# Optimization experiments

Measured on AMD Instinct MI355X. Metric: run time of the kernel, lower is better.

Reference implementation:

```python
import jax, jax.numpy as jnp
from jax import lax
import numpy as np

B, S, E = 512, 128, 300
NF = 100          # filters per kernel size
NUM_CLASSES = 5


def setup_inputs() -> dict:
    key = jax.random.key(0)
    ks = jax.random.split(key, 9)
    def w(k, shape, fan_in):
        bound = 1.0 / np.sqrt(fan_in)
        return jax.random.uniform(k, shape, jnp.float32, -bound, bound)
    return {
        "x":   jax.random.normal(ks[0], (B, 1, S, E), jnp.float32),
        # conv weights: [out_ch=NF, in_ch=1, kh, kw=E] (the 100 separate 1-channel
        # convs of each kernel size are stacked into one grouped weight tensor)
        "w3": w(ks[1], (NF, 1, 3, E), 3 * E),
        "b3": w(ks[2], (NF,), 3 * E),
        "w4": w(ks[3], (NF, 1, 4, E), 4 * E),
        "b4": w(ks[4], (NF,), 4 * E),
        "w5": w(ks[5], (NF, 1, 5, E), 5 * E),
        "b5": w(ks[6], (NF,), 5 * E),
        "Wfc": w(ks[7], (NUM_CLASSES, 3 * NF), 3 * NF),
        "bfc": w(ks[8], (NUM_CLASSES,), 3 * NF),
    }


def _branch(x, w, b, pad):
    # conv over [B,1,S,E] with kernel [NF,1,k,E]; width fully consumed -> out [B,NF,S',1]
    y = lax.conv_general_dilated(
        x, w, window_strides=(1, 1), padding=[(pad, pad), (0, 0)],
        dimension_numbers=("NCHW", "OIHW", "NCHW"))
    y = jax.nn.relu(y + b[None, :, None, None])
    # relu then global max-pool over the length dim == max over (S', 1)
    return jnp.max(y, axis=(2, 3))  # [B, NF]


def reference(x, w3, b3, w4, b4, w5, b5, Wfc, bfc):
    feats = jnp.concatenate(
        [_branch(x, w3, b3, 0),   # k=3, no padding
         _branch(x, w4, b4, 1),   # k=4, padding (1,0)
         _branch(x, w5, b5, 2)],  # k=5, padding (2,0)
        axis=1)                   # [B, 300]
    logits = feats @ Wfc.T + bfc  # dropout is identity in eval mode
    return jax.nn.log_softmax(logits, axis=1)
```

## Files before the change

kernel.cpp:

```cpp
#include <hip/hip_runtime.h>

typedef __bf16 bf16x8 __attribute__((ext_vector_type(8)));
typedef float  f32x4  __attribute__((ext_vector_type(4)));
typedef unsigned short u16;

#define NB    512
#define SEQ   128
#define EMB   300
#define NT_TOT 19
#define KT_TOT 50
#define WU_ELEMS (304 * 1600)
#define OFF_FEATS (WU_ELEMS * 2)

#define GRP_ELEMS 128000

#define AROW 640
#define A_BYTES (69 * AROW)

__device__ __forceinline__ u16 f2bf(float f) {
  unsigned u = __builtin_bit_cast(unsigned, f);
  return (u16)((u + 0x7fffu + ((u >> 16) & 1u)) >> 16);
}

__global__ void prep_weights(const float* __restrict__ w3, const float* __restrict__ w4,
                             const float* __restrict__ w5, u16* __restrict__ wu) {
  int idx = blockIdx.x * blockDim.x + threadIdx.x;
  if (idx >= WU_ELEMS) return;
  int j = idx & 7, l = (idx >> 3) & 63, t = idx >> 9;
  int nt = t % NT_TOT, kt = t / NT_TOT;
  int f  = nt * 16 + (l & 15);
  int kk = kt * 32 + ((l >> 4) << 3) + j;
  int dk = kk / 320, e = kk - dk * 320;
  float v = 0.f;
  if (f < 300 && e < 300) {
    if (f < 100)      { if (dk >= 2) v = w3[(f * 3 + dk - 2) * 300 + e]; }
    else if (f < 200) { if (dk >= 1) v = w4[((f - 100) * 4 + dk - 1) * 300 + e]; }
    else              {              v = w5[((f - 200) * 5 + dk) * 300 + e]; }
  }
  int g    = nt / 5;
  int tloc = nt - g * 5;
  int ntw  = (g == 3) ? 4 : 5;
  wu[g * GRP_ELEMS + (kt * ntw + tloc) * 512 + (l << 3) + j] = f2bf(v);
}

template<int NTW>
__device__ __forceinline__ void kloop_epi(const char* xs, const char* gB0,
                                          int ntb, int l, int b, int s0,
                                          const float* __restrict__ b3,
                                          const float* __restrict__ b4,
                                          const float* __restrict__ b5,
                                          float* __restrict__ feats) {
  const int lo = l & 15, hi = l >> 4;

  f32x4 acc[4][NTW];
  #pragma unroll
  for (int mt = 0; mt < 4; ++mt)
    #pragma unroll
    for (int j = 0; j < NTW; ++j) acc[mt][j] = (f32x4){0.f, 0.f, 0.f, 0.f};

  bf16x8 aa[4], bC[NTW], bN[NTW];

  const char* gB = gB0 + l * 16;
  #pragma unroll
  for (int j = 0; j < NTW; ++j) bC[j] = *reinterpret_cast<const bf16x8*>(gB + j * 1024);
  #pragma unroll
  for (int j = 0; j < NTW; ++j) bN[j] = *reinterpret_cast<const bf16x8*>(gB + (NTW + j) * 1024);
  gB += 2 * NTW * 1024;

  int abase[4];
  #pragma unroll
  for (int mt = 0; mt < 4; ++mt) abase[mt] = (mt * 16 + lo) * AROW + hi * 16;

#define STEP(AOFF, SW, Bcon) {                                                 \
    _Pragma("unroll") for (int mt = 0; mt < 4; ++mt)                           \
      aa[mt] = *reinterpret_cast<const bf16x8*>(xs + ((abase[mt] + (AOFF)) ^ (SW))); \
    _Pragma("unroll") for (int mt = 0; mt < 4; ++mt)                           \
    _Pragma("unroll") for (int j = 0; j < NTW; ++j)                            \
      acc[mt][j] = __builtin_amdgcn_mfma_f32_16x16x32_bf16(aa[mt], Bcon[j],    \
                                                           acc[mt][j], 0, 0, 0); \
    _Pragma("unroll") for (int j = 0; j < NTW; ++j)                            \
      Bcon[j] = *reinterpret_cast<const bf16x8*>(gB + j * 1024);               \
    gB += NTW * 1024; }

  #pragma unroll 1
  for (int dk = 0; dk < 5; ++dk) {
    const int sw = ((lo + dk) & 7) << 4;
    STEP(  0, sw, bC)
    STEP( 64, sw, bN)
    STEP(128, sw, bC)
    STEP(192, sw, bN)
    STEP(256, sw, bC)
    STEP(320, sw, bN)
    STEP(384, sw, bC)
    STEP(448, sw, bN)
    STEP(512, sw, bC)
    STEP(576, sw, bN)
    #pragma unroll
    for (int mt = 0; mt < 4; ++mt) abase[mt] += AROW;
  }
#undef STEP

  #pragma unroll
  for (int j = 0; j < NTW; ++j) {
    int f = (ntb + j) * 16 + lo;
    if (f < 300) {
      float bia  = (f < 100) ? b3[f] : (f < 200) ? b4[f - 100] : b5[f - 200];
      int   sval = (f < 100) ? 126   : (f < 200) ? 127         : 128;
      float cmax = 0.f;
      #pragma unroll
      for (int mt = 0; mt < 4; ++mt)
        #pragma unroll
        for (int ii = 0; ii < 4; ++ii) {
          int s = s0 + mt * 16 + hi * 4 + ii;
          float v = acc[mt][j][ii] + bia;
          if (s < sval) cmax = fmaxf(cmax, v);
        }
      cmax = fmaxf(cmax, __shfl_xor(cmax, 16));
      cmax = fmaxf(cmax, __shfl_xor(cmax, 32));
      if (hi == 0)
        atomicMax((int*)&feats[b * 300 + f], __float_as_int(fmaxf(cmax, 0.f)));
    }
  }
}

__global__ __launch_bounds__(256, 3)
void conv_max_kernel(const float* __restrict__ x, const u16* __restrict__ wu,
                     const float* __restrict__ b3, const float* __restrict__ b4,
                     const float* __restrict__ b5, float* __restrict__ feats) {
  __shared__ __align__(16) char xs[A_BYTES];
  const int bid = blockIdx.x;
  const int b = bid >> 1, s0 = (bid & 1) * 64;
  const int tid = threadIdx.x;
  const int l = tid & 63, w = tid >> 6;
  const float* xb = x + (size_t)b * (SEQ * EMB);
  const char*  wB = (const char*)wu + w * (GRP_ELEMS * 2);

  for (int t = tid; t < 68 * 80; t += 256) {
    int r = t / 80, cg = t - r * 80;
    int xr = s0 - 2 + r;
    float4 v = make_float4(0.f, 0.f, 0.f, 0.f);
    if (xr >= 0 && xr < SEQ && cg < 75)
      v = *reinterpret_cast<const float4*>(xb + xr * EMB + cg * 4);
    ushort4 h;
    h.x = f2bf(v.x); h.y = f2bf(v.y); h.z = f2bf(v.z); h.w = f2bf(v.w);
    int boff = (r * AROW + cg * 8) ^ ((r & 7) << 4);
    *reinterpret_cast<ushort4*>(xs + boff) = h;
  }
  __syncthreads();

  if (w == 3) kloop_epi<4>(xs, wB, 15, l, b, s0, b3, b4, b5, feats);
  else        kloop_epi<5>(xs, wB, w * 5, l, b, s0, b3, b4, b5, feats);
}

__global__ void fc_kernel(const float* __restrict__ feats, const float* __restrict__ Wfc,
                          const float* __restrict__ bfc, float* __restrict__ out) {
  const int b = blockIdx.x, l = threadIdx.x;
  float acc[5] = {0.f, 0.f, 0.f, 0.f, 0.f};
  for (int e = l; e < 300; e += 64) {
    float fv = feats[b * 300 + e];
    #pragma unroll
    for (int c = 0; c < 5; ++c) acc[c] += fv * Wfc[c * 300 + e];
  }
  #pragma unroll
  for (int off = 32; off; off >>= 1) {
    #pragma unroll
    for (int c = 0; c < 5; ++c) acc[c] += __shfl_down(acc[c], off);
  }
  if (l == 0) {
    float lg[5], m = -1e30f;
    #pragma unroll
    for (int c = 0; c < 5; ++c) { lg[c] = acc[c] + bfc[c]; m = fmaxf(m, lg[c]); }
    float se = 0.f;
    #pragma unroll
    for (int c = 0; c < 5; ++c) se += expf(lg[c] - m);
    float ls = logf(se);
    #pragma unroll
    for (int c = 0; c < 5; ++c) out[b * 5 + c] = lg[c] - m - ls;
  }
}

extern "C" void kernel_launch(void* const* d_in, const int* in_sizes, int n_in,
                              void* d_out, int out_size, void* d_ws, size_t ws_size,
                              hipStream_t stream) {
  const float* x   = (const float*)d_in[0];
  const float* w3  = (const float*)d_in[1];
  const float* b3  = (const float*)d_in[2];
  const float* w4  = (const float*)d_in[3];
  const float* b4  = (const float*)d_in[4];
  const float* w5  = (const float*)d_in[5];
  const float* b5  = (const float*)d_in[6];
  const float* Wfc = (const float*)d_in[7];
  const float* bfc = (const float*)d_in[8];
  float* out = (float*)d_out;

  u16*   wu    = (u16*)d_ws;
  float* feats = (float*)((char*)d_ws + OFF_FEATS);

  hipMemsetAsync(feats, 0, NB * 300 * sizeof(float), stream);

  prep_weights<<<(WU_ELEMS + 255) / 256, 256, 0, stream>>>(w3, w4, w5, wu);
  conv_max_kernel<<<NB * 2, 256, 0, stream>>>(x, wu, b3, b4, b5, feats);
  fc_kernel<<<NB, 64, 0, stream>>>(feats, Wfc, bfc, out);
}
```

Measured before the change: 81.00 us.

## Merge sequence halves into one 512-thread block with deeper weight prefetch

Each block now handles a full batch row with 8 waves (two M halves by four N groups), so the shared x tile is staged once and the two-row halo is not loaded twice. The weight register prefetch moves from two buffers to four with a fully unrolled dk loop. MFMA sections are wrapped in s_setprio, and x is read with nontemporal loads. The trade-off is lower occupancy (launch bounds 512,1), a larger LDS footprint, and more registers for the extra prefetch buffers.

```diff
diff --git a/kernel.cpp b/kernel.cpp
--- a/kernel.cpp
+++ b/kernel.cpp
@@ -2,6 +2,7 @@
 
 typedef __bf16 bf16x8 __attribute__((ext_vector_type(8)));
 typedef float  f32x4  __attribute__((ext_vector_type(4)));
+typedef float  f32x4v __attribute__((ext_vector_type(4)));
 typedef unsigned short u16;
 
 #define NB    512
@@ -15,7 +16,7 @@
 #define GRP_ELEMS 128000
 
 #define AROW 640
-#define A_BYTES (69 * AROW)
+#define A_BYTES (132 * AROW)
 
 __device__ __forceinline__ u16 f2bf(float f) {
   unsigned u = __builtin_bit_cast(unsigned, f);
@@ -44,8 +45,8 @@
 }
 
 template<int NTW>
-__device__ __forceinline__ void kloop_epi(const char* xs, const char* gB0,
-                                          int ntb, int l, int b, int s0,
+__device__ __forceinline__ void kloop_epi(const char* xs, const char* wB,
+                                          int ntb, int l, int b, int wmbase,
                                           const float* __restrict__ b3,
                                           const float* __restrict__ b4,
                                           const float* __restrict__ b5,
@@ -58,46 +59,51 @@
     #pragma unroll
     for (int j = 0; j < NTW; ++j) acc[mt][j] = (f32x4){0.f, 0.f, 0.f, 0.f};
 
-  bf16x8 aa[4], bC[NTW], bN[NTW];
-
-  const char* gB = gB0 + l * 16;
-  #pragma unroll
-  for (int j = 0; j < NTW; ++j) bC[j] = *reinterpret_cast<const bf16x8*>(gB + j * 1024);
-  #pragma unroll
-  for (int j = 0; j < NTW; ++j) bN[j] = *reinterpret_cast<const bf16x8*>(gB + (NTW + j) * 1024);
-  gB += 2 * NTW * 1024;
+  bf16x8 aa[4], b0[NTW], b1[NTW], b2[NTW], b3v[NTW];
+
+  const char* gB = wB + l * 16;
+  #pragma unroll
+  for (int j = 0; j < NTW; ++j) b0[j]  = *reinterpret_cast<const bf16x8*>(gB + j * 1024);
+  gB += NTW * 1024;
+  #pragma unroll
+  for (int j = 0; j < NTW; ++j) b1[j]  = *reinterpret_cast<const bf16x8*>(gB + j * 1024);
+  gB += NTW * 1024;
+  #pragma unroll
+  for (int j = 0; j < NTW; ++j) b2[j]  = *reinterpret_cast<const bf16x8*>(gB + j * 1024);
+  gB += NTW * 1024;
+  #pragma unroll
+  for (int j = 0; j < NTW; ++j) b3v[j] = *reinterpret_cast<const bf16x8*>(gB + j * 1024);
+  gB += NTW * 1024;
 
   int abase[4];
   #pragma unroll
-  for (int mt = 0; mt < 4; ++mt) abase[mt] = (mt * 16 + lo) * AROW + hi * 16;
-
-#define STEP(AOFF, SW, Bcon) {                                                 \
+  for (int mt = 0; mt < 4; ++mt) abase[mt] = (wmbase + mt * 16 + lo) * AROW + hi * 16;
+
+#define STEP(EG, BS) {                                                         \
     _Pragma("unroll") for (int mt = 0; mt < 4; ++mt)                           \
-      aa[mt] = *reinterpret_cast<const bf16x8*>(xs + ((abase[mt] + (AOFF)) ^ (SW))); \
+      aa[mt] = *reinterpret_cast<const bf16x8*>(xs + ((abase[mt] + (EG) * 64) ^ sw)); \
+    __builtin_amdgcn_s_setprio(1);                                             \
     _Pragma("unroll") for (int mt = 0; mt < 4; ++mt)                           \
     _Pragma("unroll") for (int j = 0; j < NTW; ++j)                            \
-      acc[mt][j] = __builtin_amdgcn_mfma_f32_16x16x32_bf16(aa[mt], Bcon[j],    \
+      acc[mt][j] = __builtin_amdgcn_mfma_f32_16x16x32_bf16(aa[mt], BS[j],      \
                                                            acc[mt][j], 0, 0, 0); \
+    __builtin_amdgcn_s_setprio(0);                                             \
     _Pragma("unroll") for (int j = 0; j < NTW; ++j)                            \
-      Bcon[j] = *reinterpret_cast<const bf16x8*>(gB + j * 1024);               \
+      BS[j] = *reinterpret_cast<const bf16x8*>(gB + j * 1024);                 \
     gB += NTW * 1024; }
 
-  #pragma unroll 1
-  for (int dk = 0; dk < 5; ++dk) {
-    const int sw = ((lo + dk) & 7) << 4;
-    STEP(  0, sw, bC)
-    STEP( 64, sw, bN)
-    STEP(128, sw, bC)
-    STEP(192, sw, bN)
-    STEP(256, sw, bC)
-    STEP(320, sw, bN)
-    STEP(384, sw, bC)
-    STEP(448, sw, bN)
-    STEP(512, sw, bC)
-    STEP(576, sw, bN)
-    #pragma unroll
-    for (int mt = 0; mt < 4; ++mt) abase[mt] += AROW;
-  }
+#define DKBODY(DK, S0,S1,S2,S3,S4,S5,S6,S7,S8,S9) {                            \
+    const int sw = ((lo + (DK)) & 7) << 4;                                     \
+    STEP(0,S0) STEP(1,S1) STEP(2,S2) STEP(3,S3) STEP(4,S4)                     \
+    STEP(5,S5) STEP(6,S6) STEP(7,S7) STEP(8,S8) STEP(9,S9)                     \
+    _Pragma("unroll") for (int mt = 0; mt < 4; ++mt) abase[mt] += AROW; }
+
+  DKBODY(0, b0,b1,b2,b3v,b0,b1,b2,b3v,b0,b1)
+  DKBODY(1, b2,b3v,b0,b1,b2,b3v,b0,b1,b2,b3v)
+  DKBODY(2, b0,b1,b2,b3v,b0,b1,b2,b3v,b0,b1)
+  DKBODY(3, b2,b3v,b0,b1,b2,b3v,b0,b1,b2,b3v)
+  DKBODY(4, b0,b1,b2,b3v,b0,b1,b2,b3v,b0,b1)
+#undef DKBODY
 #undef STEP
 
   #pragma unroll
@@ -111,7 +117,7 @@
       for (int mt = 0; mt < 4; ++mt)
         #pragma unroll
         for (int ii = 0; ii < 4; ++ii) {
-          int s = s0 + mt * 16 + hi * 4 + ii;
+          int s = wmbase + mt * 16 + hi * 4 + ii;
           float v = acc[mt][j][ii] + bia;
           if (s < sval) cmax = fmaxf(cmax, v);
         }
@@ -123,24 +129,25 @@
   }
 }
 
-__global__ __launch_bounds__(256, 3)
+__global__ __launch_bounds__(512, 1)
 void conv_max_kernel(const float* __restrict__ x, const u16* __restrict__ wu,
                      const float* __restrict__ b3, const float* __restrict__ b4,
                      const float* __restrict__ b5, float* __restrict__ feats) {
   __shared__ __align__(16) char xs[A_BYTES];
-  const int bid = blockIdx.x;
-  const int b = bid >> 1, s0 = (bid & 1) * 64;
+  const int b   = blockIdx.x;
   const int tid = threadIdx.x;
   const int l = tid & 63, w = tid >> 6;
+  const int wm = w >> 2, wn = w & 3;
   const float* xb = x + (size_t)b * (SEQ * EMB);
-  const char*  wB = (const char*)wu + w * (GRP_ELEMS * 2);
-
-  for (int t = tid; t < 68 * 80; t += 256) {
+  const char*  wB = (const char*)wu + wn * (GRP_ELEMS * 2);
+
+  for (int t = tid; t < 132 * 80; t += 512) {
     int r = t / 80, cg = t - r * 80;
-    int xr = s0 - 2 + r;
-    float4 v = make_float4(0.f, 0.f, 0.f, 0.f);
+    int xr = r - 2;
+    f32x4v v = (f32x4v){0.f, 0.f, 0.f, 0.f};
     if (xr >= 0 && xr < SEQ && cg < 75)
-      v = *reinterpret_cast<const float4*>(xb + xr * EMB + cg * 4);
+      v = __builtin_nontemporal_load(
+            reinterpret_cast<const f32x4v*>(xb + xr * EMB + cg * 4));
     ushort4 h;
     h.x = f2bf(v.x); h.y = f2bf(v.y); h.z = f2bf(v.z); h.w = f2bf(v.w);
     int boff = (r * AROW + cg * 8) ^ ((r & 7) << 4);
@@ -148,8 +155,8 @@
   }
   __syncthreads();
 
-  if (w == 3) kloop_epi<4>(xs, wB, 15, l, b, s0, b3, b4, b5, feats);
-  else        kloop_epi<5>(xs, wB, w * 5, l, b, s0, b3, b4, b5, feats);
+  if (wn == 3) kloop_epi<4>(xs, wB, 15,     l, b, wm * 64, b3, b4, b5, feats);
+  else         kloop_epi<5>(xs, wB, wn * 5, l, b, wm * 64, b3, b4, b5, feats);
 }
 
 __global__ void fc_kernel(const float* __restrict__ feats, const float* __restrict__ Wfc,
@@ -199,6 +206,6 @@
   hipMemsetAsync(feats, 0, NB * 300 * sizeof(float), stream);
 
   prep_weights<<<(WU_ELEMS + 255) / 256, 256, 0, stream>>>(w3, w4, w5, wu);
-  conv_max_kernel<<<NB * 2, 256, 0, stream>>>(x, wu, b3, b4, b5, feats);
+  conv_max_kernel<<<NB, 512, 0, stream>>>(x, wu, b3, b4, b5, feats);
   fc_kernel<<<NB, 64, 0, stream>>>(feats, Wfc, bfc, out);
 }
```

New measurement: 89.85 us. +10.9%, slower.
